# Optimization experiments

Hardware: AMD Instinct MI355X
Metric: run time of the kernel (lower is better)

The kernel has to match this reference:

```python
import jax, jax.numpy as jnp
import numpy as np

BZ, SEQ, IN_SZ, HID_SZ = 256, 512, 256, 256


def setup_inputs() -> dict:
    key = jax.random.key(0)
    k1, k2, k3, k4, k5 = jax.random.split(key, 5)
    stdv = 1.0 / np.sqrt(HID_SZ)
    return {
        "encoder_inputs": jax.random.normal(k1, (BZ, HID_SZ), dtype=jnp.float32),
        "decoder_inputs": jax.random.normal(k2, (BZ, SEQ, IN_SZ), dtype=jnp.float32),
        "U_i": jax.random.uniform(k3, (IN_SZ, HID_SZ), minval=-stdv, maxval=stdv, dtype=jnp.float32),
        "V_i": jax.random.uniform(k4, (HID_SZ, HID_SZ), minval=-stdv, maxval=stdv, dtype=jnp.float32),
        "b_i": jax.random.uniform(k5, (HID_SZ,), minval=-stdv, maxval=stdv, dtype=jnp.float32),
    }


def reference(encoder_inputs, decoder_inputs, U_i, V_i, b_i):
    # Sequential vanilla-RNN recurrence over time via lax.scan.
    # h_t = tanh(x_t @ U_i + h_{t-1} @ V_i + b_i)
    xs = jnp.swapaxes(decoder_inputs, 0, 1)  # [seq, bz, in]

    def step(h, x_t):
        h_new = jnp.tanh(x_t @ U_i + h @ V_i + b_i)
        return h_new, h_new

    _, outs = jax.lax.scan(step, encoder_inputs, xs)  # outs: [seq, bz, hid]
    decoder_outputs = jnp.swapaxes(outs, 0, 1)  # [bz, seq, hid]
    return (encoder_inputs, decoder_outputs)
```

## Files before the change

kernel.cpp:

```cpp
#include <hip/hip_runtime.h>
#include <hip/hip_bf16.h>


#define SEQn 512
#define HIDn 256

typedef __attribute__((ext_vector_type(4))) float    floatx4;
typedef __attribute__((ext_vector_type(8))) short    short8;
typedef __attribute__((ext_vector_type(8))) _Float16 half8;

#define LDS_BARRIER() asm volatile("s_waitcnt lgkmcnt(0)\n\ts_barrier" ::: "memory")

__device__ __forceinline__ short f2bf(float f) {
    __hip_bfloat16 h = __float2bfloat16(f);
    return *reinterpret_cast<short*>(&h);
}

__global__ void prep_B(const float* __restrict__ U, short* __restrict__ wsB) {
    int idx = blockIdx.x * 256 + threadIdx.x;
    int n  = idx & 255;
    int q  = (idx >> 8) & 3;
    int kb = idx >> 10;
    int k0 = kb * 32 + q * 8;
    short8 c;
    #pragma unroll
    for (int j = 0; j < 8; j++)
        c[j] = f2bf(U[(size_t)(k0 + j) * 256 + n]);
    *(short8*)(wsB + (size_t)idx * 8) = c;
}

__global__ __launch_bounds__(256, 4)
void xu_gemm(const float* __restrict__ X, const short* __restrict__ wsB,
             const float* __restrict__ bias, float* __restrict__ out)
{
    const int tid = threadIdx.x;
    const int l   = tid & 63;
    const int w   = tid >> 6;
    const int lr  = l & 15;
    const int q   = l >> 4;
    const int m0  = blockIdx.y * 128;
    const int n0  = blockIdx.x * 128;

    floatx4 acc[2][8];
    #pragma unroll
    for (int mt = 0; mt < 2; mt++)
        #pragma unroll
        for (int nt = 0; nt < 8; nt++)
            acc[mt][nt] = (floatx4){0.f, 0.f, 0.f, 0.f};

    const size_t rowA = (size_t)(m0 + 32 * w + lr);

    for (int kb = 0; kb < 8; kb++) {
        short8 af[2];
        #pragma unroll
        for (int mt = 0; mt < 2; mt++) {
            const float* p = X + (rowA + 16 * mt) * 256 + kb * 32 + q * 8;
            float4 a0 = *(const float4*)p;
            float4 a1 = *(const float4*)(p + 4);
            af[mt][0] = f2bf(a0.x); af[mt][1] = f2bf(a0.y);
            af[mt][2] = f2bf(a0.z); af[mt][3] = f2bf(a0.w);
            af[mt][4] = f2bf(a1.x); af[mt][5] = f2bf(a1.y);
            af[mt][6] = f2bf(a1.z); af[mt][7] = f2bf(a1.w);
        }
        #pragma unroll
        for (int nt = 0; nt < 8; nt++) {
            short8 bfr = *(const short8*)(wsB +
                ((size_t)(kb * 4 + q) * 256 + n0 + 16 * nt + lr) * 8);
            acc[0][nt] = __builtin_amdgcn_mfma_f32_16x16x32_bf16(af[0], bfr, acc[0][nt], 0, 0, 0);
            acc[1][nt] = __builtin_amdgcn_mfma_f32_16x16x32_bf16(af[1], bfr, acc[1][nt], 0, 0, 0);
        }
    }

    #pragma unroll
    for (int nt = 0; nt < 8; nt++) {
        float bv = bias[n0 + 16 * nt + lr];
        #pragma unroll
        for (int mt = 0; mt < 2; mt++) {
            #pragma unroll
            for (int r = 0; r < 4; r++) {
                int row = m0 + 32 * w + 16 * mt + 4 * q + r;
                out[(size_t)row * 256 + n0 + 16 * nt + lr] = acc[mt][nt][r] + bv;
            }
        }
    }
}

__global__ __launch_bounds__(512, 2)
void rnn_rec(const float* __restrict__ enc, const float* __restrict__ V,
             float* __restrict__ out)
{
    __shared__ _Float16 hbuf[2][HIDn];

    const int tid = threadIdx.x;
    const int w   = tid >> 6;
    const int l   = tid & 63;
    const int lr  = l & 15;
    const int q   = l >> 4;
    const int b   = blockIdx.x;
    const int c0  = 32 * w + lr;

    half8 vf[2][8];
    #pragma unroll
    for (int c = 0; c < 8; c++) {
        const float* vp = V + (size_t)(32 * c + 8 * q) * HIDn + 32 * w + lr;
        #pragma unroll
        for (int nt = 0; nt < 2; nt++) {
            half8 tmp;
            #pragma unroll
            for (int j = 0; j < 8; j++)
                tmp[j] = (_Float16)vp[(size_t)j * HIDn + 16 * nt];
            vf[nt][c] = tmp;
        }
    }

    float* outEnc = out + (size_t)b * HIDn;
    float* outDec = out + (size_t)65536 + (size_t)b * SEQn * HIDn;

    if (tid < HIDn) {
        float h0 = enc[(size_t)b * HIDn + tid];
        outEnc[tid]  = h0;
        hbuf[0][tid] = (_Float16)h0;
    }

    float xu_cur0 = outDec[c0];
    float xu_cur1 = outDec[c0 + 16];
    float xu_nx0  = outDec[HIDn + c0];
    float xu_nx1  = outDec[HIDn + c0 + 16];

    LDS_BARRIER();

    int p = 0;
    for (int t = 0; t < SEQn; t++) {
        float pf0 = 0.f, pf1 = 0.f;
        if (t + 2 < SEQn) {
            const float* xp = outDec + (size_t)(t + 2) * HIDn;
            pf0 = xp[c0];
            pf1 = xp[c0 + 16];
        }

        half8 af[8];
        #pragma unroll
        for (int c = 0; c < 8; c++)
            af[c] = *(const half8*)&hbuf[p][32 * c + 8 * q];

        floatx4 acc[2][4];
        #pragma unroll
        for (int nt = 0; nt < 2; nt++)
            #pragma unroll
            for (int ch = 0; ch < 4; ch++)
                acc[nt][ch] = (floatx4){0.f,0.f,0.f,0.f};
        #pragma unroll
        for (int c = 0; c < 8; c++) {
            acc[0][c & 3] = __builtin_amdgcn_mfma_f32_16x16x32_f16(af[c], vf[0][c], acc[0][c & 3], 0, 0, 0);
            acc[1][c & 3] = __builtin_amdgcn_mfma_f32_16x16x32_f16(af[c], vf[1][c], acc[1][c & 3], 0, 0, 0);
        }

        float s0 = ((acc[0][0][0] + acc[0][1][0]) + (acc[0][2][0] + acc[0][3][0])) + xu_cur0;
        float s1 = ((acc[1][0][0] + acc[1][1][0]) + (acc[1][2][0] + acc[1][3][0])) + xu_cur1;
        float e0 = __expf(2.f * s0);
        float e1 = __expf(2.f * s1);
        float hv0 = 1.f - 2.f / (e0 + 1.f);
        float hv1 = 1.f - 2.f / (e1 + 1.f);

        if (q == 0) {
            hbuf[p ^ 1][c0]      = (_Float16)hv0;
            hbuf[p ^ 1][c0 + 16] = (_Float16)hv1;
            float* op = outDec + (size_t)t * HIDn;
            op[c0]      = hv0;
            op[c0 + 16] = hv1;
        }

        xu_cur0 = xu_nx0; xu_cur1 = xu_nx1;
        xu_nx0  = pf0;    xu_nx1  = pf1;
        p ^= 1;
        LDS_BARRIER();
    }
}

extern "C" void kernel_launch(void* const* d_in, const int* in_sizes, int n_in,
                              void* d_out, int out_size, void* d_ws, size_t ws_size,
                              hipStream_t stream) {
    const float* enc  = (const float*)d_in[0];
    const float* x    = (const float*)d_in[1];
    const float* U    = (const float*)d_in[2];
    const float* V    = (const float*)d_in[3];
    const float* bias = (const float*)d_in[4];
    float* out = (float*)d_out;

    float* outDec = out + 65536;

    short* wsB = (ws_size >= 131072) ? (short*)d_ws : (short*)out;

    prep_B<<<32, 256, 0, stream>>>(U, wsB);

    dim3 ggrid(2, 1024);
    xu_gemm<<<ggrid, 256, 0, stream>>>(x, wsB, bias, outDec);

    rnn_rec<<<256, 512, 0, stream>>>(enc, V, out);
}
```

Before: 547.7 us.

## Stage X tiles in swizzled LDS and split recurrence over K with partial sums

The input-projection GEMM now has each block cover all 256 output columns, so X is read once rather than twice. X tiles are double-buffered through XOR-swizzled LDS while the next tile is prefetched into registers. The recurrent kernel drops from 512 to 256 threads per batch row: each wave handles a 64-wide K slice across all 16 N tiles, and the four waves reduce their partial sums through LDS. This costs an extra barrier per timestep in exchange for fewer idle lanes and one output per thread.

New measurement: 610.7 us. 1.11x slower.

```diff
diff --git a/kernel.cpp b/kernel.cpp
--- a/kernel.cpp
+++ b/kernel.cpp
@@ -29,67 +29,98 @@
     *(short8*)(wsB + (size_t)idx * 8) = c;
 }
 
-__global__ __launch_bounds__(256, 4)
+__global__ __launch_bounds__(256, 2)
 void xu_gemm(const float* __restrict__ X, const short* __restrict__ wsB,
              const float* __restrict__ bias, float* __restrict__ out)
 {
+    __shared__ float Xlds[2][4096];
+
     const int tid = threadIdx.x;
     const int l   = tid & 63;
     const int w   = tid >> 6;
     const int lr  = l & 15;
     const int q   = l >> 4;
-    const int m0  = blockIdx.y * 128;
-    const int n0  = blockIdx.x * 128;
-
-    floatx4 acc[2][8];
+    const int m0  = blockIdx.x * 128;
+
+    const int srow = tid >> 3;
+    const int sgrp = (tid & 7) ^ (srow & 7);
+    const float* xbase = X + (size_t)(m0 + srow) * 256 + 4 * sgrp;
+
+    floatx4 acc[2][16];
     #pragma unroll
     for (int mt = 0; mt < 2; mt++)
         #pragma unroll
-        for (int nt = 0; nt < 8; nt++)
+        for (int nt = 0; nt < 16; nt++)
             acc[mt][nt] = (floatx4){0.f, 0.f, 0.f, 0.f};
 
-    const size_t rowA = (size_t)(m0 + 32 * w + lr);
-
+    float4 st[4];
+    #pragma unroll
+    for (int j = 0; j < 4; j++)
+        st[j] = *(const float4*)(xbase + (size_t)(32 * j) * 256);
+    #pragma unroll
+    for (int j = 0; j < 4; j++)
+        *(float4*)&Xlds[0][j * 1024 + 4 * tid] = st[j];
+    LDS_BARRIER();
+
+    #pragma unroll
     for (int kb = 0; kb < 8; kb++) {
+        const int cur = kb & 1;
+        if (kb < 7) {
+            #pragma unroll
+            for (int j = 0; j < 4; j++)
+                st[j] = *(const float4*)(xbase + (size_t)(32 * j) * 256 + (kb + 1) * 32);
+        }
+
         short8 af[2];
         #pragma unroll
         for (int mt = 0; mt < 2; mt++) {
-            const float* p = X + (rowA + 16 * mt) * 256 + kb * 32 + q * 8;
-            float4 a0 = *(const float4*)p;
-            float4 a1 = *(const float4*)(p + 4);
+            const int row = 32 * w + 16 * mt + lr;
+            const int g0 = (2 * q) ^ (row & 7);
+            const int g1 = (2 * q + 1) ^ (row & 7);
+            float4 a0 = *(const float4*)&Xlds[cur][row * 32 + 4 * g0];
+            float4 a1 = *(const float4*)&Xlds[cur][row * 32 + 4 * g1];
             af[mt][0] = f2bf(a0.x); af[mt][1] = f2bf(a0.y);
             af[mt][2] = f2bf(a0.z); af[mt][3] = f2bf(a0.w);
             af[mt][4] = f2bf(a1.x); af[mt][5] = f2bf(a1.y);
             af[mt][6] = f2bf(a1.z); af[mt][7] = f2bf(a1.w);
         }
-        #pragma unroll
-        for (int nt = 0; nt < 8; nt++) {
+
+        #pragma unroll
+        for (int nt = 0; nt < 16; nt++) {
             short8 bfr = *(const short8*)(wsB +
-                ((size_t)(kb * 4 + q) * 256 + n0 + 16 * nt + lr) * 8);
+                ((size_t)(kb * 4 + q) * 256 + 16 * nt + lr) * 8);
             acc[0][nt] = __builtin_amdgcn_mfma_f32_16x16x32_bf16(af[0], bfr, acc[0][nt], 0, 0, 0);
             acc[1][nt] = __builtin_amdgcn_mfma_f32_16x16x32_bf16(af[1], bfr, acc[1][nt], 0, 0, 0);
         }
-    }
-
-    #pragma unroll
-    for (int nt = 0; nt < 8; nt++) {
-        float bv = bias[n0 + 16 * nt + lr];
+
+        if (kb < 7) {
+            #pragma unroll
+            for (int j = 0; j < 4; j++)
+                *(float4*)&Xlds[cur ^ 1][j * 1024 + 4 * tid] = st[j];
+        }
+        LDS_BARRIER();
+    }
+
+    #pragma unroll
+    for (int nt = 0; nt < 16; nt++) {
+        float bv = bias[16 * nt + lr];
         #pragma unroll
         for (int mt = 0; mt < 2; mt++) {
             #pragma unroll
             for (int r = 0; r < 4; r++) {
                 int row = m0 + 32 * w + 16 * mt + 4 * q + r;
-                out[(size_t)row * 256 + n0 + 16 * nt + lr] = acc[mt][nt][r] + bv;
+                out[(size_t)row * 256 + 16 * nt + lr] = acc[mt][nt][r] + bv;
             }
         }
     }
 }
 
-__global__ __launch_bounds__(512, 2)
+__global__ __launch_bounds__(256, 1)
 void rnn_rec(const float* __restrict__ enc, const float* __restrict__ V,
              float* __restrict__ out)
 {
     __shared__ _Float16 hbuf[2][HIDn];
+    __shared__ float    part[4][HIDn];
 
     const int tid = threadIdx.x;
     const int w   = tid >> 6;
@@ -97,18 +128,17 @@
     const int lr  = l & 15;
     const int q   = l >> 4;
     const int b   = blockIdx.x;
-    const int c0  = 32 * w + lr;
-
-    half8 vf[2][8];
-    #pragma unroll
-    for (int c = 0; c < 8; c++) {
-        const float* vp = V + (size_t)(32 * c + 8 * q) * HIDn + 32 * w + lr;
-        #pragma unroll
-        for (int nt = 0; nt < 2; nt++) {
+
+    half8 vf[16][2];
+    #pragma unroll
+    for (int nt = 0; nt < 16; nt++) {
+        #pragma unroll
+        for (int c = 0; c < 2; c++) {
+            const float* vp = V + (size_t)(64 * w + 32 * c + 8 * q) * HIDn + 16 * nt + lr;
             half8 tmp;
             #pragma unroll
             for (int j = 0; j < 8; j++)
-                tmp[j] = (_Float16)vp[(size_t)j * HIDn + 16 * nt];
+                tmp[j] = (_Float16)vp[(size_t)j * HIDn];
             vf[nt][c] = tmp;
         }
     }
@@ -116,62 +146,52 @@
     float* outEnc = out + (size_t)b * HIDn;
     float* outDec = out + (size_t)65536 + (size_t)b * SEQn * HIDn;
 
-    if (tid < HIDn) {
+    {
         float h0 = enc[(size_t)b * HIDn + tid];
         outEnc[tid]  = h0;
         hbuf[0][tid] = (_Float16)h0;
     }
 
-    float xu_cur0 = outDec[c0];
-    float xu_cur1 = outDec[c0 + 16];
-    float xu_nx0  = outDec[HIDn + c0];
-    float xu_nx1  = outDec[HIDn + c0 + 16];
+    float xu_cur = outDec[tid];
+    float xu_nx  = outDec[HIDn + tid];
+
+    const floatx4 zero4 = {0.f, 0.f, 0.f, 0.f};
 
     LDS_BARRIER();
 
     int p = 0;
     for (int t = 0; t < SEQn; t++) {
-        float pf0 = 0.f, pf1 = 0.f;
-        if (t + 2 < SEQn) {
-            const float* xp = outDec + (size_t)(t + 2) * HIDn;
-            pf0 = xp[c0];
-            pf1 = xp[c0 + 16];
-        }
-
-        half8 af[8];
-        #pragma unroll
-        for (int c = 0; c < 8; c++)
-            af[c] = *(const half8*)&hbuf[p][32 * c + 8 * q];
-
-        floatx4 acc[2][4];
-        #pragma unroll
-        for (int nt = 0; nt < 2; nt++)
-            #pragma unroll
-            for (int ch = 0; ch < 4; ch++)
-                acc[nt][ch] = (floatx4){0.f,0.f,0.f,0.f};
-        #pragma unroll
-        for (int c = 0; c < 8; c++) {
-            acc[0][c & 3] = __builtin_amdgcn_mfma_f32_16x16x32_f16(af[c], vf[0][c], acc[0][c & 3], 0, 0, 0);
-            acc[1][c & 3] = __builtin_amdgcn_mfma_f32_16x16x32_f16(af[c], vf[1][c], acc[1][c & 3], 0, 0, 0);
-        }
-
-        float s0 = ((acc[0][0][0] + acc[0][1][0]) + (acc[0][2][0] + acc[0][3][0])) + xu_cur0;
-        float s1 = ((acc[1][0][0] + acc[1][1][0]) + (acc[1][2][0] + acc[1][3][0])) + xu_cur1;
-        float e0 = __expf(2.f * s0);
-        float e1 = __expf(2.f * s1);
-        float hv0 = 1.f - 2.f / (e0 + 1.f);
-        float hv1 = 1.f - 2.f / (e1 + 1.f);
-
-        if (q == 0) {
-            hbuf[p ^ 1][c0]      = (_Float16)hv0;
-            hbuf[p ^ 1][c0 + 16] = (_Float16)hv1;
-            float* op = outDec + (size_t)t * HIDn;
-            op[c0]      = hv0;
-            op[c0 + 16] = hv1;
-        }
-
-        xu_cur0 = xu_nx0; xu_cur1 = xu_nx1;
-        xu_nx0  = pf0;    xu_nx1  = pf1;
+        float pf = 0.f;
+        if (t + 2 < SEQn) pf = outDec[(size_t)(t + 2) * HIDn + tid];
+
+        half8 af0 = *(const half8*)&hbuf[p][64 * w + 8 * q];
+        half8 af1 = *(const half8*)&hbuf[p][64 * w + 32 + 8 * q];
+
+        floatx4 acc[16];
+        #pragma unroll
+        for (int nt = 0; nt < 16; nt++) {
+            floatx4 a = __builtin_amdgcn_mfma_f32_16x16x32_f16(af0, vf[nt][0], zero4, 0, 0, 0);
+            acc[nt]   = __builtin_amdgcn_mfma_f32_16x16x32_f16(af1, vf[nt][1], a,     0, 0, 0);
+        }
+
+        #pragma unroll
+        for (int i = 0; i < 4; i++) {
+            float v01 = (q & 1) ? acc[4 + i][0]  : acc[i][0];
+            float v23 = (q & 1) ? acc[12 + i][0] : acc[8 + i][0];
+            float v   = (q & 2) ? v23 : v01;
+            part[w][64 * q + 16 * i + lr] = v;
+        }
+
+        LDS_BARRIER();
+
+        float s = (part[0][tid] + part[1][tid]) + (part[2][tid] + part[3][tid]) + xu_cur;
+        float e = __expf(2.f * s);
+        float h = 1.f - __fdividef(2.f, e + 1.f);
+        hbuf[p ^ 1][tid] = (_Float16)h;
+        outDec[(size_t)t * HIDn + tid] = h;
+
+        xu_cur = xu_nx;
+        xu_nx  = pf;
         p ^= 1;
         LDS_BARRIER();
     }
@@ -193,8 +213,7 @@
 
     prep_B<<<32, 256, 0, stream>>>(U, wsB);
 
-    dim3 ggrid(2, 1024);
-    xu_gemm<<<ggrid, 256, 0, stream>>>(x, wsB, bias, outDec);
-
-    rnn_rec<<<256, 512, 0, stream>>>(enc, V, out);
-}
+    xu_gemm<<<1024, 256, 0, stream>>>(x, wsB, bias, outDec);
+
+    rnn_rec<<<256, 256, 0, stream>>>(enc, V, out);
+}
```

## Fuse input projection GEMM into recurrent kernel with per-chunk LDS staging

Applied to the files above, without the earlier changes.

Drops the separate weight-prep and X·U GEMM kernels. Each recurrent block now loads 64-timestep chunks of its batch row's inputs into a swizzled fp16 LDS tile and computes X·U+bias with MFMA into an LDS buffer, then runs the 64 recurrent steps reading from it. This avoids writing the full XU intermediate to global memory and reading it back, and saves two launches. In exchange it uses fp16 instead of bf16 for X·U, holds U fragments in registers alongside V, and adds a per-chunk GEMM phase that sits on the serial critical path with only 256 blocks. The tanh division now uses __fdividef.

New measurement: 486.2 us. 11.2% less time.

```diff
diff --git a/kernel.cpp b/kernel.cpp
--- a/kernel.cpp
+++ b/kernel.cpp
@@ -2,93 +2,23 @@
 #include <hip/hip_bf16.h>
 
 
-#define SEQn 512
-#define HIDn 256
+#define SEQn   512
+#define HIDn   256
+#define CHUNK  64
+#define NCHUNK 8
 
 typedef __attribute__((ext_vector_type(4))) float    floatx4;
-typedef __attribute__((ext_vector_type(8))) short    short8;
 typedef __attribute__((ext_vector_type(8))) _Float16 half8;
 
 #define LDS_BARRIER() asm volatile("s_waitcnt lgkmcnt(0)\n\ts_barrier" ::: "memory")
 
-__device__ __forceinline__ short f2bf(float f) {
-    __hip_bfloat16 h = __float2bfloat16(f);
-    return *reinterpret_cast<short*>(&h);
-}
-
-__global__ void prep_B(const float* __restrict__ U, short* __restrict__ wsB) {
-    int idx = blockIdx.x * 256 + threadIdx.x;
-    int n  = idx & 255;
-    int q  = (idx >> 8) & 3;
-    int kb = idx >> 10;
-    int k0 = kb * 32 + q * 8;
-    short8 c;
-    #pragma unroll
-    for (int j = 0; j < 8; j++)
-        c[j] = f2bf(U[(size_t)(k0 + j) * 256 + n]);
-    *(short8*)(wsB + (size_t)idx * 8) = c;
-}
-
-__global__ __launch_bounds__(256, 4)
-void xu_gemm(const float* __restrict__ X, const short* __restrict__ wsB,
-             const float* __restrict__ bias, float* __restrict__ out)
+__global__ __launch_bounds__(512, 1)
+void rnn_fused(const float* __restrict__ enc, const float* __restrict__ x,
+               const float* __restrict__ U,   const float* __restrict__ V,
+               const float* __restrict__ bias, float* __restrict__ out)
 {
-    const int tid = threadIdx.x;
-    const int l   = tid & 63;
-    const int w   = tid >> 6;
-    const int lr  = l & 15;
-    const int q   = l >> 4;
-    const int m0  = blockIdx.y * 128;
-    const int n0  = blockIdx.x * 128;
-
-    floatx4 acc[2][8];
-    #pragma unroll
-    for (int mt = 0; mt < 2; mt++)
-        #pragma unroll
-        for (int nt = 0; nt < 8; nt++)
-            acc[mt][nt] = (floatx4){0.f, 0.f, 0.f, 0.f};
-
-    const size_t rowA = (size_t)(m0 + 32 * w + lr);
-
-    for (int kb = 0; kb < 8; kb++) {
-        short8 af[2];
-        #pragma unroll
-        for (int mt = 0; mt < 2; mt++) {
-            const float* p = X + (rowA + 16 * mt) * 256 + kb * 32 + q * 8;
-            float4 a0 = *(const float4*)p;
-            float4 a1 = *(const float4*)(p + 4);
-            af[mt][0] = f2bf(a0.x); af[mt][1] = f2bf(a0.y);
-            af[mt][2] = f2bf(a0.z); af[mt][3] = f2bf(a0.w);
-            af[mt][4] = f2bf(a1.x); af[mt][5] = f2bf(a1.y);
-            af[mt][6] = f2bf(a1.z); af[mt][7] = f2bf(a1.w);
-        }
-        #pragma unroll
-        for (int nt = 0; nt < 8; nt++) {
-            short8 bfr = *(const short8*)(wsB +
-                ((size_t)(kb * 4 + q) * 256 + n0 + 16 * nt + lr) * 8);
-            acc[0][nt] = __builtin_amdgcn_mfma_f32_16x16x32_bf16(af[0], bfr, acc[0][nt], 0, 0, 0);
-            acc[1][nt] = __builtin_amdgcn_mfma_f32_16x16x32_bf16(af[1], bfr, acc[1][nt], 0, 0, 0);
-        }
-    }
-
-    #pragma unroll
-    for (int nt = 0; nt < 8; nt++) {
-        float bv = bias[n0 + 16 * nt + lr];
-        #pragma unroll
-        for (int mt = 0; mt < 2; mt++) {
-            #pragma unroll
-            for (int r = 0; r < 4; r++) {
-                int row = m0 + 32 * w + 16 * mt + 4 * q + r;
-                out[(size_t)row * 256 + n0 + 16 * nt + lr] = acc[mt][nt][r] + bv;
-            }
-        }
-    }
-}
-
-__global__ __launch_bounds__(512, 2)
-void rnn_rec(const float* __restrict__ enc, const float* __restrict__ V,
-             float* __restrict__ out)
-{
+    __shared__ _Float16 xbf[CHUNK][HIDn];
+    __shared__ float    xu[CHUNK][HIDn + 1];
     __shared__ _Float16 hbuf[2][HIDn];
 
     const int tid = threadIdx.x;
@@ -99,81 +29,124 @@
     const int b   = blockIdx.x;
     const int c0  = 32 * w + lr;
 
-    half8 vf[2][8];
+    half8 uf[2][8], vf[2][8];
     #pragma unroll
     for (int c = 0; c < 8; c++) {
-        const float* vp = V + (size_t)(32 * c + 8 * q) * HIDn + 32 * w + lr;
+        const float* up = U + (size_t)(32 * c + 8 * q) * HIDn + c0;
+        const float* vp = V + (size_t)(32 * c + 8 * q) * HIDn + c0;
         #pragma unroll
         for (int nt = 0; nt < 2; nt++) {
-            half8 tmp;
+            half8 tu, tv;
             #pragma unroll
-            for (int j = 0; j < 8; j++)
-                tmp[j] = (_Float16)vp[(size_t)j * HIDn + 16 * nt];
-            vf[nt][c] = tmp;
+            for (int j = 0; j < 8; j++) {
+                tu[j] = (_Float16)up[(size_t)j * HIDn + 16 * nt];
+                tv[j] = (_Float16)vp[(size_t)j * HIDn + 16 * nt];
+            }
+            uf[nt][c] = tu;
+            vf[nt][c] = tv;
         }
     }
 
-    float* outEnc = out + (size_t)b * HIDn;
-    float* outDec = out + (size_t)65536 + (size_t)b * SEQn * HIDn;
+    const float b0 = bias[c0];
+    const float b1 = bias[c0 + 16];
 
     if (tid < HIDn) {
         float h0 = enc[(size_t)b * HIDn + tid];
-        outEnc[tid]  = h0;
+        out[(size_t)b * HIDn + tid] = h0;
         hbuf[0][tid] = (_Float16)h0;
     }
 
-    float xu_cur0 = outDec[c0];
-    float xu_cur1 = outDec[c0 + 16];
-    float xu_nx0  = outDec[HIDn + c0];
-    float xu_nx1  = outDec[HIDn + c0 + 16];
+    const float* xb = x + (size_t)b * SEQn * HIDn;
+    float* outDec   = out + (size_t)65536 + (size_t)b * SEQn * HIDn;
 
-    LDS_BARRIER();
+    const int srow = tid >> 3;
+    const int scol = (tid & 7) * 32;
+
+    const floatx4 zf = {0.f, 0.f, 0.f, 0.f};
 
     int p = 0;
-    for (int t = 0; t < SEQn; t++) {
-        float pf0 = 0.f, pf1 = 0.f;
-        if (t + 2 < SEQn) {
-            const float* xp = outDec + (size_t)(t + 2) * HIDn;
-            pf0 = xp[c0];
-            pf1 = xp[c0 + 16];
+    for (int g = 0; g < NCHUNK; g++) {
+        const float* xs = xb + (size_t)(g * CHUNK + srow) * HIDn + scol;
+        float4 xv[8];
+        #pragma unroll
+        for (int i = 0; i < 8; i++)
+            xv[i] = *(const float4*)(xs + 4 * i);
+        #pragma unroll
+        for (int gi = 0; gi < 4; gi++) {
+            half8 t;
+            t[0] = (_Float16)xv[2*gi].x;   t[1] = (_Float16)xv[2*gi].y;
+            t[2] = (_Float16)xv[2*gi].z;   t[3] = (_Float16)xv[2*gi].w;
+            t[4] = (_Float16)xv[2*gi+1].x; t[5] = (_Float16)xv[2*gi+1].y;
+            t[6] = (_Float16)xv[2*gi+1].z; t[7] = (_Float16)xv[2*gi+1].w;
+            int grp = ((tid & 7) * 4 + gi) ^ (srow & 7);
+            *(half8*)&xbf[srow][grp * 8] = t;
         }
+        LDS_BARRIER();
 
-        half8 af[8];
-        #pragma unroll
-        for (int c = 0; c < 8; c++)
-            af[c] = *(const half8*)&hbuf[p][32 * c + 8 * q];
+        {
+            floatx4 ga[2][4];
+            #pragma unroll
+            for (int c = 0; c < 8; c++) {
+                half8 am[4];
+                #pragma unroll
+                for (int mt = 0; mt < 4; mt++) {
+                    int row = 16 * mt + lr;
+                    int grp = (4 * c + q) ^ (row & 7);
+                    am[mt] = *(const half8*)&xbf[row][grp * 8];
+                }
+                #pragma unroll
+                for (int mt = 0; mt < 4; mt++) {
+                    ga[0][mt] = __builtin_amdgcn_mfma_f32_16x16x32_f16(
+                        am[mt], uf[0][c], c ? ga[0][mt] : zf, 0, 0, 0);
+                    ga[1][mt] = __builtin_amdgcn_mfma_f32_16x16x32_f16(
+                        am[mt], uf[1][c], c ? ga[1][mt] : zf, 0, 0, 0);
+                }
+            }
+            #pragma unroll
+            for (int mt = 0; mt < 4; mt++)
+                #pragma unroll
+                for (int r = 0; r < 4; r++) {
+                    int row = 16 * mt + 4 * q + r;
+                    xu[row][c0]      = ga[0][mt][r] + b0;
+                    xu[row][c0 + 16] = ga[1][mt][r] + b1;
+                }
+        }
+        LDS_BARRIER();
 
-        floatx4 acc[2][4];
-        #pragma unroll
-        for (int nt = 0; nt < 2; nt++)
+        for (int tt = 0; tt < CHUNK; tt++) {
+            half8 af[8];
             #pragma unroll
-            for (int ch = 0; ch < 4; ch++)
-                acc[nt][ch] = (floatx4){0.f,0.f,0.f,0.f};
-        #pragma unroll
-        for (int c = 0; c < 8; c++) {
-            acc[0][c & 3] = __builtin_amdgcn_mfma_f32_16x16x32_f16(af[c], vf[0][c], acc[0][c & 3], 0, 0, 0);
-            acc[1][c & 3] = __builtin_amdgcn_mfma_f32_16x16x32_f16(af[c], vf[1][c], acc[1][c & 3], 0, 0, 0);
+            for (int c = 0; c < 8; c++)
+                af[c] = *(const half8*)&hbuf[p][32 * c + 8 * q];
+
+            floatx4 acc[2][4];
+            #pragma unroll
+            for (int c = 0; c < 8; c++) {
+                acc[0][c & 3] = __builtin_amdgcn_mfma_f32_16x16x32_f16(
+                    af[c], vf[0][c], (c < 4) ? zf : acc[0][c & 3], 0, 0, 0);
+                acc[1][c & 3] = __builtin_amdgcn_mfma_f32_16x16x32_f16(
+                    af[c], vf[1][c], (c < 4) ? zf : acc[1][c & 3], 0, 0, 0);
+            }
+
+            float s0 = ((acc[0][0][0] + acc[0][1][0]) + (acc[0][2][0] + acc[0][3][0]))
+                       + xu[tt][c0];
+            float s1 = ((acc[1][0][0] + acc[1][1][0]) + (acc[1][2][0] + acc[1][3][0]))
+                       + xu[tt][c0 + 16];
+            float e0  = __expf(2.f * s0);
+            float e1  = __expf(2.f * s1);
+            float hv0 = 1.f - __fdividef(2.f, e0 + 1.f);
+            float hv1 = 1.f - __fdividef(2.f, e1 + 1.f);
+
+            if (q == 0) {
+                hbuf[p ^ 1][c0]      = (_Float16)hv0;
+                hbuf[p ^ 1][c0 + 16] = (_Float16)hv1;
+                float* op = outDec + (size_t)(g * CHUNK + tt) * HIDn;
+                op[c0]      = hv0;
+                op[c0 + 16] = hv1;
+            }
+            p ^= 1;
+            LDS_BARRIER();
         }
-
-        float s0 = ((acc[0][0][0] + acc[0][1][0]) + (acc[0][2][0] + acc[0][3][0])) + xu_cur0;
-        float s1 = ((acc[1][0][0] + acc[1][1][0]) + (acc[1][2][0] + acc[1][3][0])) + xu_cur1;
-        float e0 = __expf(2.f * s0);
-        float e1 = __expf(2.f * s1);
-        float hv0 = 1.f - 2.f / (e0 + 1.f);
-        float hv1 = 1.f - 2.f / (e1 + 1.f);
-
-        if (q == 0) {
-            hbuf[p ^ 1][c0]      = (_Float16)hv0;
-            hbuf[p ^ 1][c0 + 16] = (_Float16)hv1;
-            float* op = outDec + (size_t)t * HIDn;
-            op[c0]      = hv0;
-            op[c0 + 16] = hv1;
-        }
-
-        xu_cur0 = xu_nx0; xu_cur1 = xu_nx1;
-        xu_nx0  = pf0;    xu_nx1  = pf1;
-        p ^= 1;
-        LDS_BARRIER();
     }
 }
 
@@ -187,14 +160,5 @@
     const float* bias = (const float*)d_in[4];
     float* out = (float*)d_out;
 
-    float* outDec = out + 65536;
-
-    short* wsB = (ws_size >= 131072) ? (short*)d_ws : (short*)out;
-
-    prep_B<<<32, 256, 0, stream>>>(U, wsB);
-
-    dim3 ggrid(2, 1024);
-    xu_gemm<<<ggrid, 256, 0, stream>>>(x, wsB, bias, outDec);
-
-    rnn_rec<<<256, 512, 0, stream>>>(enc, V, out);
+    rnn_fused<<<256, 512, 0, stream>>>(enc, x, U, V, bias, out);
 }
```
